# Performance work log

Hardware: AMD Instinct MI355X
Metric: run time of the kernel (lower is better)

The kernel has to match this reference:

```python
import jax, jax.numpy as jnp
import numpy as np

N, F, D, K = 4096, 128, 64, 2  # nodes, in_dim, out_dim, hops


def setup_inputs() -> dict:
    key = jax.random.key(0)
    k_x, k_a, k_e, k_w = jax.random.split(key, 4)
    X = jax.random.normal(k_x, (N, F), jnp.float32)
    # K+1 non-negative dense adjacency/distance matrices (stacked list)
    A = jax.random.uniform(k_a, (K + 1, N, N), jnp.float32)
    # Dense(out_dim, use_bias=False) weights, glorot-like scale
    W_emb = jax.random.normal(k_e, (F, D), jnp.float32) / np.sqrt(F)
    W_hops = jax.random.normal(k_w, (K + 1, F, D), jnp.float32) / np.sqrt(F)
    alpha = jnp.float32(0.1)
    return {"X": X, "A": A, "W_emb": W_emb, "W_hops": W_hops, "alpha": alpha}


def reference(X, A, W_emb, W_hops, alpha):
    # learned embeddings E = Dense(X)  -> [N, D]
    E = X @ W_emb
    # shared low-rank update alpha * E @ E^T  -> [N, N]
    low_rank = alpha * (E @ E.T)
    # per-hop kernel projections Dense_k(X)  -> [K+1, N, D]
    XW = jnp.einsum('nf,kfd->knd', X, W_hops)
    out = jnp.zeros((N, D), X.dtype)
    for k in range(A.shape[0]):  # fixed small K+1 hops
        A_hat = A[k] + low_rank                       # [N, N]
        deg = jnp.sum(A_hat, axis=1)                  # row sums
        d = jnp.power(deg, -0.5)                      # D^{-1/2}
        # D^{-1/2} A_hat D^{-1/2} via broadcast scaling (same math as diag matmuls)
        A_norm = d[:, None] * A_hat * d[None, :]
        out = out + A_norm @ XW[k]
    return jax.nn.relu(out)
```

## Files before the change

kernel.cpp:

```cpp
#include <hip/hip_runtime.h>
#include <math.h>

#define N_ 4096
#define F_ 128
#define D_ 64
#define KH_ 3
#define ZS_ 4
#define KC_ (N_ / ZS_)

#define OFF_E      0
#define OFF_XW     (N_*D_)
#define OFF_SE     (OFF_XW + KH_*N_*D_)
#define OFF_T      (OFF_SE + D_)
#define OFF_DVEC   (OFF_T + KH_*D_*D_)
#define OFF_YT     (OFF_DVEC + KH_*N_)
#define OFF_AYP    (OFF_YT + KH_*D_*N_/2)

typedef __attribute__((ext_vector_type(8))) short bf16x8;
typedef __attribute__((ext_vector_type(4))) float f32x4;

static __device__ __forceinline__ unsigned short f2bf(float f) {
  union { float f; unsigned u; } v; v.f = f;
  unsigned r = (v.u + 0x7fffu + ((v.u >> 16) & 1u)) >> 16;
  return (unsigned short)r;
}

__global__ __launch_bounds__(256) void proj_kernel(
    const float* __restrict__ X, const float* __restrict__ W_emb,
    const float* __restrict__ W_hops, float* __restrict__ ws)
{
  __shared__ __align__(16) float sXT[32][68];
  __shared__ __align__(16) float sW[32][68];
  const int t = threadIdx.x;
  const int m = blockIdx.y;
  const int row0 = blockIdx.x * 64;
  const float* W = (m == 0) ? W_emb : (W_hops + (size_t)(m - 1) * F_ * D_);
  float* out = (m == 0) ? (ws + OFF_E) : (ws + OFF_XW + (size_t)(m - 1) * N_ * D_);
  const int tx = t & 15, ty = t >> 4;
  const int d0 = tx * 4, i0 = ty * 4;
  float acc[4][4] = {};
  for (int fc = 0; fc < F_; fc += 32) {
    {
      int i_l = t >> 3;
      int f_l = (t & 7) * 4;
      for (int r = 0; r < 2; ++r) {
        int i = i_l + r * 32;
        float4 v = *(const float4*)(X + (size_t)(row0 + i) * F_ + fc + f_l);
        sXT[f_l + 0][i] = v.x; sXT[f_l + 1][i] = v.y;
        sXT[f_l + 2][i] = v.z; sXT[f_l + 3][i] = v.w;
      }
      int f2 = t >> 4;
      int d  = (t & 15) * 4;
      for (int r = 0; r < 2; ++r) {
        int f = f2 + r * 16;
        *(float4*)&sW[f][d] = *(const float4*)(W + (size_t)(fc + f) * D_ + d);
      }
    }
    __syncthreads();
#pragma unroll 8
    for (int f = 0; f < 32; ++f) {
      float a[4], b[4];
      *(float4*)a = *(const float4*)&sXT[f][i0];
      *(float4*)b = *(const float4*)&sW[f][d0];
      for (int x = 0; x < 4; ++x)
        for (int y = 0; y < 4; ++y)
          acc[x][y] += a[x] * b[y];
    }
    __syncthreads();
  }
  for (int x = 0; x < 4; ++x)
    *(float4*)(out + (size_t)(row0 + i0 + x) * D_ + d0) = *(float4*)acc[x];
  if (m == 0) {
    float p[4];
    for (int y = 0; y < 4; ++y)
      p[y] = acc[0][y] + acc[1][y] + acc[2][y] + acc[3][y];
    *(float4*)&sXT[ty][d0] = *(float4*)p;
    __syncthreads();
    if (ty < 4) {
      int c = ty * 16 + tx;
      float s = 0.f;
#pragma unroll
      for (int r = 0; r < 16; ++r) s += sXT[r][c];
      atomicAdd(ws + OFF_SE + c, s);
    }
  }
}

__global__ __launch_bounds__(256) void degree_kernel(
    const float* __restrict__ A, const float* __restrict__ E,
    const float* __restrict__ S, const float* __restrict__ alpha_p,
    float* __restrict__ dvec)
{
  int lane = threadIdx.x & 63;
  int wave = threadIdx.x >> 6;
  int row = blockIdx.x * 4 + wave;
  int i = row & (N_ - 1);
  const float4* Ar = (const float4*)(A + (size_t)row * N_);
  float s = 0.f;
#pragma unroll
  for (int it = 0; it < 16; ++it) {
    float4 v = Ar[lane + it * 64];
    s += (v.x + v.y) + (v.z + v.w);
  }
  float alpha = *alpha_p;
  s += alpha * E[(size_t)i * D_ + lane] * S[lane];
#pragma unroll
  for (int off = 32; off > 0; off >>= 1)
    s += __shfl_xor(s, off);
  if (lane == 0) dvec[row] = 1.0f / sqrtf(s);
}

__global__ __launch_bounds__(256) void prep_kernel(float* __restrict__ ws,
                                                   float* __restrict__ T)
{
  const int k = blockIdx.y;
  const float* XWk = ws + OFF_XW + (size_t)k * N_ * D_;
  const float* dk  = ws + OFF_DVEC + (size_t)k * N_;
  int t = threadIdx.x;

  if (blockIdx.x < 64) {
    const int j0 = blockIdx.x * 64;
    unsigned short* Ytk = (unsigned short*)(ws + OFF_YT) + (size_t)k * D_ * N_;
    __shared__ float sT[64][65];
    {
      int j = t >> 2;
      int c0 = (t & 3) * 16;
      float dv = dk[j0 + j];
      for (int r = 0; r < 4; ++r) {
        float4 v = *(const float4*)(XWk + (size_t)(j0 + j) * D_ + c0 + 4 * r);
        sT[c0 + 4 * r + 0][j] = v.x * dv;
        sT[c0 + 4 * r + 1][j] = v.y * dv;
        sT[c0 + 4 * r + 2][j] = v.z * dv;
        sT[c0 + 4 * r + 3][j] = v.w * dv;
      }
    }
    __syncthreads();
    {
      int n = t >> 2;
      int jq = (t & 3) * 16;
      __align__(16) unsigned short buf[16];
#pragma unroll
      for (int i = 0; i < 16; ++i) buf[i] = f2bf(sT[n][jq + i]);
      uint4* dst = (uint4*)(Ytk + (size_t)n * N_ + j0 + jq);
      dst[0] = *(uint4*)&buf[0];
      dst[1] = *(uint4*)&buf[8];
    }
  } else {
    const float* E = ws + OFF_E;
    __shared__ __align__(16) float sE[32][68];
    __shared__ __align__(16) float sY[32][68];
    int tx = t & 15, ty = t >> 4;
    int d0 = tx * 4, c0 = ty * 4;
    float acc[4][4] = {};
    int base0 = (blockIdx.x - 64) * 128;
    for (int sub = 0; sub < 4; ++sub) {
      int base = base0 + sub * 32;
      {
        int i_l = t >> 3;
        int c   = (t & 7) * 4;
        float dv = dk[base + i_l];
        for (int r = 0; r < 2; ++r) {
          int col = c + r * 32;
          *(float4*)&sE[i_l][col] = *(const float4*)(E + (size_t)(base + i_l) * D_ + col);
          float4 y = *(const float4*)(XWk + (size_t)(base + i_l) * D_ + col);
          y.x *= dv; y.y *= dv; y.z *= dv; y.w *= dv;
          *(float4*)&sY[i_l][col] = y;
        }
      }
      __syncthreads();
#pragma unroll 8
      for (int i = 0; i < 32; ++i) {
        float c4[4], y4[4];
        *(float4*)c4 = *(const float4*)&sE[i][c0];
        *(float4*)y4 = *(const float4*)&sY[i][d0];
        for (int a = 0; a < 4; ++a)
          for (int b = 0; b < 4; ++b)
            acc[a][b] += c4[a] * y4[b];
      }
      __syncthreads();
    }
    float* Tk = T + (size_t)k * D_ * D_;
    for (int a = 0; a < 4; ++a)
      for (int b = 0; b < 4; ++b)
        atomicAdd(&Tk[(c0 + a) * D_ + d0 + b], acc[a][b]);
  }
}

__global__ __launch_bounds__(256) void agemm_kernel(
    const float* __restrict__ A, const float* __restrict__ ws,
    float* __restrict__ AYp)
{
  const int k = blockIdx.y;
  const int row0 = blockIdx.x * 64;
  const int kz0 = blockIdx.z * KC_;
  const float* Ak = A + ((size_t)k << 24);
  const unsigned short* Ytk = (const unsigned short*)(ws + OFF_YT) + (size_t)k * D_ * N_;

  __shared__ __align__(16) unsigned short sA[64][72];
  __shared__ __align__(16) unsigned short sY[64][72];

  const int t = threadIdx.x;
  const int lane = t & 63;
  const int w = t >> 6;
  const int m = lane & 15;
  const int q = lane >> 4;

  f32x4 acc[4];
#pragma unroll
  for (int i = 0; i < 4; ++i) acc[i] = (f32x4){0.f, 0.f, 0.f, 0.f};

  const int ar  = t >> 2;
  const int akq = (t & 3) * 16;

  for (int kt = 0; kt < KC_; kt += 64) {
    {
      const float* gA = Ak + (size_t)(row0 + ar) * N_ + kz0 + kt + akq;
#pragma unroll
      for (int r = 0; r < 4; ++r) {
        float4 v = *(const float4*)(gA + 4 * r);
        ushort4 u;
        u.x = f2bf(v.x); u.y = f2bf(v.y); u.z = f2bf(v.z); u.w = f2bf(v.w);
        *(ushort4*)&sA[ar][akq + 4 * r] = u;
      }
      const uint4* gY = (const uint4*)(Ytk + (size_t)ar * N_ + kz0 + kt + akq);
      *(uint4*)&sY[ar][akq + 0] = gY[0];
      *(uint4*)&sY[ar][akq + 8] = gY[1];
    }
    __syncthreads();
    const int mrow = w * 16 + m;
#pragma unroll
    for (int s = 0; s < 2; ++s) {
      bf16x8 af = *(const bf16x8*)&sA[mrow][s * 32 + q * 8];
#pragma unroll
      for (int nt = 0; nt < 4; ++nt) {
        bf16x8 bfv = *(const bf16x8*)&sY[nt * 16 + m][s * 32 + q * 8];
        acc[nt] = __builtin_amdgcn_mfma_f32_16x16x32_bf16(af, bfv, acc[nt], 0, 0, 0);
      }
    }
    __syncthreads();
  }
  float* outp = AYp + (((size_t)blockIdx.z * KH_ + k) * N_ + row0 + w * 16) * D_;
#pragma unroll
  for (int nt = 0; nt < 4; ++nt)
#pragma unroll
    for (int r = 0; r < 4; ++r)
      outp[(size_t)(q * 4 + r) * D_ + nt * 16 + m] = acc[nt][r];
}

__global__ __launch_bounds__(256) void epilogue_kernel(
    const float* __restrict__ ws, const float* __restrict__ alpha_p,
    float* __restrict__ out)
{
  int g = blockIdx.x * 256 + threadIdx.x;
  int i = g >> 6, d = g & 63;
  const float* E    = ws + OFF_E;
  const float* T    = ws + OFF_T;
  const float* dvec = ws + OFF_DVEC;
  const float* AYp  = ws + OFF_AYP;
  float alpha = *alpha_p;
  float s = 0.f;
  for (int k = 0; k < KH_; ++k) {
    float ay = 0.f;
#pragma unroll
    for (int jc = 0; jc < ZS_; ++jc)
      ay += AYp[(((size_t)jc * KH_ + k) * N_ + i) * D_ + d];
    float lr = 0.f;
    const float* Tk = T + k * D_ * D_;
#pragma unroll 16
    for (int c = 0; c < D_; ++c)
      lr += E[(size_t)i * D_ + c] * Tk[c * D_ + d];
    s += dvec[k * N_ + i] * (ay + alpha * lr);
  }
  out[g] = fmaxf(s, 0.f);
}

extern "C" void kernel_launch(void* const* d_in, const int* in_sizes, int n_in,
                              void* d_out, int out_size, void* d_ws, size_t ws_size,
                              hipStream_t stream) {
  const float* X      = (const float*)d_in[0];
  const float* A      = (const float*)d_in[1];
  const float* W_emb  = (const float*)d_in[2];
  const float* W_hops = (const float*)d_in[3];
  const float* alpha_p= (const float*)d_in[4];
  float* out = (float*)d_out;
  float* ws  = (float*)d_ws;

  hipMemsetAsync(ws + OFF_SE, 0, (D_ + KH_ * D_ * D_) * sizeof(float), stream);

  proj_kernel<<<dim3(N_ / 64, 4), 256, 0, stream>>>(X, W_emb, W_hops, ws);
  degree_kernel<<<dim3(KH_ * N_ / 4), 256, 0, stream>>>(A, ws + OFF_E, ws + OFF_SE,
                                                        alpha_p, ws + OFF_DVEC);
  prep_kernel<<<dim3(96, KH_), 256, 0, stream>>>(ws, ws + OFF_T);
  agemm_kernel<<<dim3(N_ / 64, KH_, ZS_), 256, 0, stream>>>(A, ws, ws + OFF_AYP);
  epilogue_kernel<<<dim3(N_ * D_ / 256), 256, 0, stream>>>(ws, alpha_p, out);
}
```

Measured before the change: 357.0 us.

## Convert A to bf16 during degree pass and use direct-to-LDS loads in GEMM

The degree kernel now writes a bf16 copy of A while computing row sums, so the A·Y GEMM reads half the bytes. The GEMM loads tiles straight into LDS with global_load_lds into an XOR-swizzled layout. It uses 256-row tiles with a 4x4 MFMA register block per wave and raises the split-K factor to 16. This costs an extra 100MB bf16 write plus a larger partial-sum buffer, and the epilogue has to reduce more split-K partials.

New measurement: 373.0 us. 4.5% more time.

```diff
diff --git a/kernel.cpp b/kernel.cpp
--- a/kernel.cpp
+++ b/kernel.cpp
@@ -5,8 +5,9 @@
 #define F_ 128
 #define D_ 64
 #define KH_ 3
-#define ZS_ 4
+#define ZS_ 16
 #define KC_ (N_ / ZS_)
+#define BM_ 256
 
 #define OFF_E      0
 #define OFF_XW     (N_*D_)
@@ -15,6 +16,7 @@
 #define OFF_DVEC   (OFF_T + KH_*D_*D_)
 #define OFF_YT     (OFF_DVEC + KH_*N_)
 #define OFF_AYP    (OFF_YT + KH_*D_*N_/2)
+#define OFF_ABF    (OFF_AYP + ZS_*KH_*N_*D_)
 
 typedef __attribute__((ext_vector_type(8))) short bf16x8;
 typedef __attribute__((ext_vector_type(4))) float f32x4;
@@ -23,6 +25,13 @@
   union { float f; unsigned u; } v; v.f = f;
   unsigned r = (v.u + 0x7fffu + ((v.u >> 16) & 1u)) >> 16;
   return (unsigned short)r;
+}
+
+static __device__ __forceinline__ void gload_lds16(const unsigned short* g,
+                                                   unsigned short* l) {
+  __builtin_amdgcn_global_load_lds(
+      (__attribute__((address_space(1))) unsigned int*)g,
+      (__attribute__((address_space(3))) unsigned int*)l, 16, 0, 0);
 }
 
 __global__ __launch_bounds__(256) void proj_kernel(
@@ -86,21 +95,29 @@
   }
 }
 
-__global__ __launch_bounds__(256) void degree_kernel(
+__global__ __launch_bounds__(256) void degconv_kernel(
     const float* __restrict__ A, const float* __restrict__ E,
     const float* __restrict__ S, const float* __restrict__ alpha_p,
-    float* __restrict__ dvec)
+    float* __restrict__ dvec, unsigned short* __restrict__ Abf)
 {
   int lane = threadIdx.x & 63;
   int wave = threadIdx.x >> 6;
   int row = blockIdx.x * 4 + wave;
   int i = row & (N_ - 1);
   const float4* Ar = (const float4*)(A + (size_t)row * N_);
+  unsigned short* Br = Abf + (size_t)row * N_;
   float s = 0.f;
 #pragma unroll
-  for (int it = 0; it < 16; ++it) {
-    float4 v = Ar[lane + it * 64];
-    s += (v.x + v.y) + (v.z + v.w);
+  for (int it = 0; it < 8; ++it) {
+    float4 v0 = Ar[it * 128 + lane * 2 + 0];
+    float4 v1 = Ar[it * 128 + lane * 2 + 1];
+    s += (v0.x + v0.y) + (v0.z + v0.w) + (v1.x + v1.y) + (v1.z + v1.w);
+    union { unsigned short u[8]; uint4 q; } pk;
+    pk.u[0] = f2bf(v0.x); pk.u[1] = f2bf(v0.y);
+    pk.u[2] = f2bf(v0.z); pk.u[3] = f2bf(v0.w);
+    pk.u[4] = f2bf(v1.x); pk.u[5] = f2bf(v1.y);
+    pk.u[6] = f2bf(v1.z); pk.u[7] = f2bf(v1.w);
+    *(uint4*)(Br + (size_t)it * 512 + lane * 8) = pk.q;
   }
   float alpha = *alpha_p;
   s += alpha * E[(size_t)i * D_ + lane] * S[lane];
@@ -186,65 +203,77 @@
   }
 }
 
-__global__ __launch_bounds__(256) void agemm_kernel(
-    const float* __restrict__ A, const float* __restrict__ ws,
-    float* __restrict__ AYp)
+__global__ __launch_bounds__(256, 3) void agemm_kernel(
+    const float* __restrict__ ws, float* __restrict__ AYp)
 {
   const int k = blockIdx.y;
-  const int row0 = blockIdx.x * 64;
+  const int row0 = blockIdx.x * BM_;
   const int kz0 = blockIdx.z * KC_;
-  const float* Ak = A + ((size_t)k << 24);
+  const unsigned short* Ak = (const unsigned short*)(ws + OFF_ABF) + ((size_t)k << 24);
   const unsigned short* Ytk = (const unsigned short*)(ws + OFF_YT) + (size_t)k * D_ * N_;
 
-  __shared__ __align__(16) unsigned short sA[64][72];
-  __shared__ __align__(16) unsigned short sY[64][72];
+  __shared__ __align__(16) unsigned short sA[BM_ * 64];
+  __shared__ __align__(16) unsigned short sY[64 * 64];
 
   const int t = threadIdx.x;
   const int lane = t & 63;
   const int w = t >> 6;
   const int m = lane & 15;
   const int q = lane >> 4;
-
-  f32x4 acc[4];
-#pragma unroll
-  for (int i = 0; i < 4; ++i) acc[i] = (f32x4){0.f, 0.f, 0.f, 0.f};
-
-  const int ar  = t >> 2;
-  const int akq = (t & 3) * 16;
+  const int sr = t >> 3;
+  const int sc = t & 7;
+
+  f32x4 acc[4][4];
+#pragma unroll
+  for (int a = 0; a < 4; ++a)
+#pragma unroll
+    for (int b = 0; b < 4; ++b) acc[a][b] = (f32x4){0.f, 0.f, 0.f, 0.f};
 
   for (int kt = 0; kt < KC_; kt += 64) {
-    {
-      const float* gA = Ak + (size_t)(row0 + ar) * N_ + kz0 + kt + akq;
-#pragma unroll
-      for (int r = 0; r < 4; ++r) {
-        float4 v = *(const float4*)(gA + 4 * r);
-        ushort4 u;
-        u.x = f2bf(v.x); u.y = f2bf(v.y); u.z = f2bf(v.z); u.w = f2bf(v.w);
-        *(ushort4*)&sA[ar][akq + 4 * r] = u;
-      }
-      const uint4* gY = (const uint4*)(Ytk + (size_t)ar * N_ + kz0 + kt + akq);
-      *(uint4*)&sY[ar][akq + 0] = gY[0];
-      *(uint4*)&sY[ar][akq + 8] = gY[1];
-    }
-    __syncthreads();
-    const int mrow = w * 16 + m;
+#pragma unroll
+    for (int j = 0; j < 8; ++j) {
+      int r = j * 32 + sr;
+      gload_lds16(Ak + (size_t)(row0 + r) * N_ + (kz0 + kt) + ((sc ^ (r & 7)) << 3),
+                  &sA[j * 2048 + t * 8]);
+    }
+#pragma unroll
+    for (int j = 0; j < 2; ++j) {
+      int r = j * 32 + sr;
+      gload_lds16(Ytk + (size_t)r * N_ + (kz0 + kt) + ((sc ^ (r & 7)) << 3),
+                  &sY[j * 2048 + t * 8]);
+    }
+    __syncthreads();
 #pragma unroll
     for (int s = 0; s < 2; ++s) {
-      bf16x8 af = *(const bf16x8*)&sA[mrow][s * 32 + q * 8];
+      bf16x8 av[4], bv[4];
+#pragma unroll
+      for (int mr = 0; mr < 4; ++mr) {
+        int row = w * 64 + mr * 16 + m;
+        av[mr] = *(const bf16x8*)&sA[row * 64 + (((s * 4 + q) ^ (row & 7)) << 3)];
+      }
 #pragma unroll
       for (int nt = 0; nt < 4; ++nt) {
-        bf16x8 bfv = *(const bf16x8*)&sY[nt * 16 + m][s * 32 + q * 8];
-        acc[nt] = __builtin_amdgcn_mfma_f32_16x16x32_bf16(af, bfv, acc[nt], 0, 0, 0);
-      }
-    }
-    __syncthreads();
-  }
-  float* outp = AYp + (((size_t)blockIdx.z * KH_ + k) * N_ + row0 + w * 16) * D_;
-#pragma unroll
-  for (int nt = 0; nt < 4; ++nt)
-#pragma unroll
-    for (int r = 0; r < 4; ++r)
-      outp[(size_t)(q * 4 + r) * D_ + nt * 16 + m] = acc[nt][r];
+        int n = nt * 16 + m;
+        bv[nt] = *(const bf16x8*)&sY[n * 64 + (((s * 4 + q) ^ (n & 7)) << 3)];
+      }
+#pragma unroll
+      for (int mr = 0; mr < 4; ++mr)
+#pragma unroll
+        for (int nt = 0; nt < 4; ++nt)
+          acc[mr][nt] = __builtin_amdgcn_mfma_f32_16x16x32_bf16(av[mr], bv[nt],
+                                                                acc[mr][nt], 0, 0, 0);
+    }
+    __syncthreads();
+  }
+#pragma unroll
+  for (int mr = 0; mr < 4; ++mr) {
+    float* outp = AYp + (((size_t)blockIdx.z * KH_ + k) * N_ + row0 + w * 64 + mr * 16) * D_;
+#pragma unroll
+    for (int nt = 0; nt < 4; ++nt)
+#pragma unroll
+      for (int r = 0; r < 4; ++r)
+        outp[(size_t)(q * 4 + r) * D_ + nt * 16 + m] = acc[mr][nt][r];
+  }
 }
 
 __global__ __launch_bounds__(256) void epilogue_kernel(
@@ -288,9 +317,10 @@
   hipMemsetAsync(ws + OFF_SE, 0, (D_ + KH_ * D_ * D_) * sizeof(float), stream);
 
   proj_kernel<<<dim3(N_ / 64, 4), 256, 0, stream>>>(X, W_emb, W_hops, ws);
-  degree_kernel<<<dim3(KH_ * N_ / 4), 256, 0, stream>>>(A, ws + OFF_E, ws + OFF_SE,
-                                                        alpha_p, ws + OFF_DVEC);
+  degconv_kernel<<<dim3(KH_ * N_ / 4), 256, 0, stream>>>(
+      A, ws + OFF_E, ws + OFF_SE, alpha_p, ws + OFF_DVEC,
+      (unsigned short*)(ws + OFF_ABF));
   prep_kernel<<<dim3(96, KH_), 256, 0, stream>>>(ws, ws + OFF_T);
-  agemm_kernel<<<dim3(N_ / 64, KH_, ZS_), 256, 0, stream>>>(A, ws, ws + OFF_AYP);
+  agemm_kernel<<<dim3(N_ / BM_, KH_, ZS_), 256, 0, stream>>>(ws, ws + OFF_AYP);
   epilogue_kernel<<<dim3(N_ * D_ / 256), 256, 0, stream>>>(ws, alpha_p, out);
 }
```
